# Optimization experiments

Hardware: AMD Instinct MI355X
Metric: run time of the kernel (lower is better)

The kernel has to match this reference:

```python
import jax, jax.numpy as jnp
import numpy as np

HIDDEN = 1024
HEADS = 16
HEAD_DIM = HIDDEN // HEADS


def setup_inputs() -> dict:
    key = jax.random.key(0)
    ks = jax.random.split(key, 4)
    B, S, H = 2, 2048, HIDDEN
    scale = 1.0 / np.sqrt(H)
    return {
        "inputs": jax.random.normal(ks[0], (B, S, H), dtype=jnp.float32),
        "mask": jnp.ones((B, S), dtype=jnp.int32),
        "Wq": jax.random.normal(ks[1], (H, H), dtype=jnp.float32) * scale,
        "bq": jnp.zeros((H,), dtype=jnp.float32),
        "Wk": jax.random.normal(ks[2], (H, H), dtype=jnp.float32) * scale,
        "bk": jnp.zeros((H,), dtype=jnp.float32),
        "Wv": jax.random.normal(ks[3], (H, H), dtype=jnp.float32) * scale,
        "bv": jnp.zeros((H,), dtype=jnp.float32),
    }


def _split_heads(x, B, S):
    # [B,S,H] -> [B,heads,S,head_dim]
    return x.reshape(B, S, HEADS, HEAD_DIM).transpose(0, 2, 1, 3)


def reference(inputs, mask, Wq, bq, Wk, bk, Wv, bv):
    B, S, H = inputs.shape
    q = _split_heads(inputs @ Wq.T + bq, B, S)
    k = _split_heads(inputs @ Wk.T + bk, B, S)
    v = _split_heads(inputs @ Wv.T + bv, B, S)
    scores = jnp.einsum("bhqd,bhkd->bhqk", q, k) / jnp.sqrt(
        jnp.asarray(HEAD_DIM, dtype=inputs.dtype))
    # mask broadcast [B,1,1,S]; zeros -> -inf
    scores = jnp.where(mask[:, None, None, :] == 0, -jnp.inf, scores)
    attn = jax.nn.softmax(scores, axis=-1)
    context = jnp.einsum("bhqk,bhkd->bhqd", attn, v)
    return context.transpose(0, 2, 1, 3).reshape(B, S, H)
```

## Files before the change

kernel.cpp:

```cpp
#include <hip/hip_runtime.h>
#include <hip/hip_fp16.h>

constexpr int S_LEN  = 2048;
constexpr int HID    = 1024;
constexpr int HEADS  = 16;
constexpr int HDIM   = 64;
constexpr int BATCH  = 2;
constexpr int BH     = BATCH * HEADS;
constexpr int M_ROWS = BATCH * S_LEN;

typedef _Float16 half8  __attribute__((ext_vector_type(8)));
typedef _Float16 half4v __attribute__((ext_vector_type(4)));
typedef _Float16 half2v __attribute__((ext_vector_type(2)));
typedef float    f32x4  __attribute__((ext_vector_type(4)));
typedef float    f32x16 __attribute__((ext_vector_type(16)));

constexpr float EXP2_OFF = -11.541560327111707f;
constexpr float Q_SCALE  = 0.18033688011112042f;

__global__ __launch_bounds__(256) void cvt_kernel(
    const float* __restrict__ X,  const float* __restrict__ Wq,
    const float* __restrict__ Wk, const float* __restrict__ Wv,
    const int* __restrict__ mask,
    _Float16* __restrict__ Xh,  _Float16* __restrict__ Wqh,
    _Float16* __restrict__ Wkh, _Float16* __restrict__ Wvh,
    float* __restrict__ maskF)
{
    const int blk = blockIdx.x;
    if (blk >= 3584) {
        const int loc = blk - 3584;
        const size_t e = ((size_t)loc * 256 + threadIdx.x) * 8;
        #pragma unroll
        for (int i = 0; i < 8; ++i)
            maskF[e + i] = mask[e + i] ? EXP2_OFF : -1.0e30f;
        return;
    }
    const float* src; _Float16* dst; int loc;
    if (blk < 2048)      { src = X;  dst = Xh;  loc = blk; }
    else if (blk < 2560) { src = Wq; dst = Wqh; loc = blk - 2048; }
    else if (blk < 3072) { src = Wk; dst = Wkh; loc = blk - 2560; }
    else                 { src = Wv; dst = Wvh; loc = blk - 3072; }
    const size_t e = ((size_t)loc * 256 + threadIdx.x) * 8;
    float4 a = *reinterpret_cast<const float4*>(&src[e]);
    float4 b = *reinterpret_cast<const float4*>(&src[e + 4]);
    half8 h = { (_Float16)a.x, (_Float16)a.y, (_Float16)a.z, (_Float16)a.w,
                (_Float16)b.x, (_Float16)b.y, (_Float16)b.z, (_Float16)b.w };
    *reinterpret_cast<half8*>(&dst[e]) = h;
}

__device__ __forceinline__ void async_cp16(_Float16* lds, const _Float16* g) {
    __builtin_amdgcn_global_load_lds(
        (const __attribute__((address_space(1))) void*)g,
        (__attribute__((address_space(3))) void*)lds, 16, 0, 0);
}

__global__ __launch_bounds__(256) void qkv_proj_kernel(
    const _Float16* __restrict__ Xh,
    const _Float16* __restrict__ Wqh, const _Float16* __restrict__ Wkh,
    const _Float16* __restrict__ Wvh,
    const float* __restrict__ bq, const float* __restrict__ bk,
    const float* __restrict__ bv,
    _Float16* __restrict__ Qo, _Float16* __restrict__ Ko,
    _Float16* __restrict__ Vt)
{
    const int mode = blockIdx.z;
    const _Float16* W    = (mode == 0) ? Wqh : (mode == 1) ? Wkh : Wvh;
    const float*    bias = (mode == 0) ? bq  : (mode == 1) ? bk  : bv;

    const int m0 = blockIdx.x * 128, n0 = blockIdx.y * 128;
    const int tid = threadIdx.x, wave = tid >> 6, lane = tid & 63;
    const int l31 = lane & 31, kg = lane >> 5;

    __shared__ _Float16 SMEM[18432];

    f32x16 acc[2][2];
    #pragma unroll
    for (int mt = 0; mt < 2; ++mt)
        #pragma unroll
        for (int nt = 0; nt < 2; ++nt)
            #pragma unroll
            for (int i = 0; i < 16; ++i) acc[mt][nt][i] = 0.f;

    const int wm = (wave & 1) * 64, wn = (wave >> 1) * 64;

    const int srow = tid >> 2, spos = tid & 3;
    auto stage = [&](int k0, int b) {
        _Float16* Asb = SMEM + b * 8192;
        _Float16* Bsb = Asb + 4096;
        #pragma unroll
        for (int j = 0; j < 2; ++j) {
            const int row = srow + j * 64;
            const int sch = spos ^ (row & 3);
            async_cp16(&Asb[j * 2048 + tid * 8],
                       &Xh[(size_t)(m0 + row) * HID + k0 + sch * 8]);
            async_cp16(&Bsb[j * 2048 + tid * 8],
                       &W [(size_t)(n0 + row) * HID + k0 + sch * 8]);
        }
    };

    stage(0, 0);
    int buf = 0;

    for (int k0 = 0; k0 < HID; k0 += 32) {
        __syncthreads();
        if (k0 + 32 < HID) stage(k0 + 32, buf ^ 1);
        _Float16* Asb = SMEM + buf * 8192;
        _Float16* Bsb = Asb + 4096;

        #pragma unroll
        for (int c = 0; c < 2; ++c) {
            const int k8 = c * 2 + kg;
            half8 af[2], bf[2];
            #pragma unroll
            for (int mt = 0; mt < 2; ++mt) {
                const int row = wm + mt * 32 + l31;
                af[mt] = *reinterpret_cast<const half8*>(
                    &Asb[row * 32 + ((k8 ^ (row & 3)) * 8)]);
            }
            #pragma unroll
            for (int nt = 0; nt < 2; ++nt) {
                const int row = wn + nt * 32 + l31;
                bf[nt] = *reinterpret_cast<const half8*>(
                    &Bsb[row * 32 + ((k8 ^ (row & 3)) * 8)]);
            }
            #pragma unroll
            for (int mt = 0; mt < 2; ++mt)
                #pragma unroll
                for (int nt = 0; nt < 2; ++nt)
                    acc[mt][nt] = __builtin_amdgcn_mfma_f32_32x32x16_f16(
                        af[mt], bf[nt], acc[mt][nt], 0, 0, 0);
        }
        buf ^= 1;
    }
    __syncthreads();

    _Float16* T = SMEM + wave * 4608;

    const int nn  = n0 + wn;
    const int hh  = nn >> 6;
    const int mm  = m0 + wm;
    const int bb  = mm >> 11;
    const int bhv = bb * HEADS + hh;
    const int s0  = mm & 2047;
    const int rowg = lane >> 3, chunk = lane & 7;

    if (mode < 2) {
        _Float16* Out = (mode == 0) ? Qo : Ko;
        #pragma unroll
        for (int nt = 0; nt < 2; ++nt) {
            const int col = nt * 32 + l31;
            float bias_n = bias[nn + col];
            #pragma unroll
            for (int mt = 0; mt < 2; ++mt)
                #pragma unroll
                for (int r = 0; r < 16; ++r) {
                    const int row_l = (r & 3) + 8 * (r >> 2) + 4 * kg;
                    float v = acc[mt][nt][r] + bias_n;
                    if (mode == 0) v *= Q_SCALE;
                    T[(mt * 32 + row_l) * 72 + col] = (_Float16)v;
                }
        }
        asm volatile("s_waitcnt lgkmcnt(0)" ::: "memory");
        #pragma unroll
        for (int j = 0; j < 8; ++j) {
            const int sr = j * 8 + rowg;
            half8 v = *reinterpret_cast<const half8*>(&T[sr * 72 + chunk * 8]);
            *reinterpret_cast<half8*>(
                &Out[((size_t)bhv * S_LEN + s0 + sr) * HDIM + chunk * 8]) = v;
        }
    } else {
        #pragma unroll
        for (int nt = 0; nt < 2; ++nt) {
            const int col = nt * 32 + l31;
            const float bias_n = bias[nn + col];
            #pragma unroll
            for (int mt = 0; mt < 2; ++mt)
                #pragma unroll
                for (int rg = 0; rg < 4; ++rg) {
                    half4v t = { (_Float16)(acc[mt][nt][rg * 4 + 0] + bias_n),
                                 (_Float16)(acc[mt][nt][rg * 4 + 1] + bias_n),
                                 (_Float16)(acc[mt][nt][rg * 4 + 2] + bias_n),
                                 (_Float16)(acc[mt][nt][rg * 4 + 3] + bias_n) };
                    const int s_off = mt * 32 + 8 * rg + 4 * kg;
                    *reinterpret_cast<half4v*>(&T[col * 72 + s_off]) = t;
                }
        }
        asm volatile("s_waitcnt lgkmcnt(0)" ::: "memory");
        #pragma unroll
        for (int j = 0; j < 8; ++j) {
            const int dr = j * 8 + rowg;
            half8 v = *reinterpret_cast<const half8*>(&T[dr * 72 + chunk * 8]);
            *reinterpret_cast<half8*>(
                &Vt[((size_t)bhv * HDIM + dr) * S_LEN + s0 + chunk * 8]) = v;
        }
    }
}

__global__ __launch_bounds__(512) void attn_kernel(
    const _Float16* __restrict__ Q, const _Float16* __restrict__ K,
    const _Float16* __restrict__ Vt, const float* __restrict__ maskF,
    float* __restrict__ Out)
{
    const int id    = blockIdx.x;
    const int xcd   = id & 7, local = id >> 3;
    const int bh    = xcd * 4 + (local & 3);
    const int qt    = local >> 2;
    const int b = bh >> 4, h = bh & 15;
    const int tid = threadIdx.x, wave = tid >> 6, lane = tid & 63;
    const int l15 = lane & 15, quad = lane >> 4;

    __shared__ _Float16 Ks[2][64 * 64];
    __shared__ _Float16 Vs[2][64 * 64];
    __shared__ _Float16 Ps[8][16][68];

    const _Float16* Qb = Q  + (size_t)bh * S_LEN * HDIM;
    const _Float16* Kb = K  + (size_t)bh * S_LEN * HDIM;
    const _Float16* Vb = Vt + (size_t)bh * HDIM * S_LEN;
    const float*    mb = maskF + b * S_LEN;

    const int qrow = qt * 128 + wave * 16 + l15;
    half8 qf[2];
    qf[0] = *reinterpret_cast<const half8*>(&Qb[(size_t)qrow * HDIM + quad * 8]);
    qf[1] = *reinterpret_cast<const half8*>(&Qb[(size_t)qrow * HDIM + 32 + quad * 8]);

    f32x4 acc[4];
    #pragma unroll
    for (int mt = 0; mt < 4; ++mt) acc[mt] = (f32x4){0.f, 0.f, 0.f, 0.f};
    float den = 0.f;

    const int srow_t  = tid >> 3;
    const int schunk  = (tid & 7) ^ (srow_t & 7);
    auto stage = [&](int kb, int buf) {
        async_cp16(&Ks[buf][tid * 8],
                   &Kb[(size_t)(kb + srow_t) * HDIM + schunk * 8]);
        async_cp16(&Vs[buf][tid * 8],
                   &Vb[(size_t)srow_t * S_LEN + kb + schunk * 8]);
    };

    stage(0, 0);
    int buf = 0;
    const int rsw = (l15 & 7);

    for (int kb = 0; kb < S_LEN; kb += 64) {
        __syncthreads();
        if (kb + 64 < S_LEN) stage(kb + 64, buf ^ 1);

        float4 m4[4];
        #pragma unroll
        for (int nt = 0; nt < 4; ++nt)
            m4[nt] = *reinterpret_cast<const float4*>(&mb[kb + nt * 16 + quad * 4]);

        half8 kf[2][4];
        #pragma unroll
        for (int c = 0; c < 2; ++c)
            #pragma unroll
            for (int nt = 0; nt < 4; ++nt)
                kf[c][nt] = *reinterpret_cast<const half8*>(
                    &Ks[buf][(nt * 16 + l15) * 64 + ((c * 4 + quad) ^ rsw) * 8]);
        f32x4 sc[4];
        #pragma unroll
        for (int nt = 0; nt < 4; ++nt) sc[nt] = (f32x4){0.f, 0.f, 0.f, 0.f};
        #pragma unroll
        for (int c = 0; c < 2; ++c)
            #pragma unroll
            for (int nt = 0; nt < 4; ++nt)
                sc[nt] = __builtin_amdgcn_mfma_f32_16x16x32_f16(
                    kf[c][nt], qf[c], sc[nt], 0, 0, 0);

        half8 vf[2][4];
        #pragma unroll
        for (int c = 0; c < 2; ++c)
            #pragma unroll
            for (int mt = 0; mt < 4; ++mt)
                vf[c][mt] = *reinterpret_cast<const half8*>(
                    &Vs[buf][(mt * 16 + l15) * 64 + ((c * 4 + quad) ^ rsw) * 8]);

        #pragma unroll
        for (int nt = 0; nt < 4; ++nt) {
            float p0 = __builtin_amdgcn_exp2f(sc[nt][0] + m4[nt].x);
            float p1 = __builtin_amdgcn_exp2f(sc[nt][1] + m4[nt].y);
            float p2 = __builtin_amdgcn_exp2f(sc[nt][2] + m4[nt].z);
            float p3 = __builtin_amdgcn_exp2f(sc[nt][3] + m4[nt].w);
            den += (p0 + p1) + (p2 + p3);
            half2v lo = __builtin_bit_cast(half2v, __builtin_amdgcn_cvt_pkrtz(p0, p1));
            half2v hi = __builtin_bit_cast(half2v, __builtin_amdgcn_cvt_pkrtz(p2, p3));
            half4v pk = { lo[0], lo[1], hi[0], hi[1] };
            *reinterpret_cast<half4v*>(&Ps[wave][l15][nt * 16 + quad * 4]) = pk;
        }
        asm volatile("s_waitcnt lgkmcnt(0)" ::: "memory");

        #pragma unroll
        for (int c = 0; c < 2; ++c) {
            half4v plo = *reinterpret_cast<const half4v*>(
                &Ps[wave][l15][c * 32 + quad * 8]);
            half4v phi = *reinterpret_cast<const half4v*>(
                &Ps[wave][l15][c * 32 + quad * 8 + 4]);
            half8 pf = { plo[0], plo[1], plo[2], plo[3],
                         phi[0], phi[1], phi[2], phi[3] };
            #pragma unroll
            for (int mt = 0; mt < 4; ++mt)
                acc[mt] = __builtin_amdgcn_mfma_f32_16x16x32_f16(
                    vf[c][mt], pf, acc[mt], 0, 0, 0);
        }
        buf ^= 1;
    }

    den += __shfl_xor(den, 16, 64);
    den += __shfl_xor(den, 32, 64);
    const float inv = 1.0f / den;

    float* orow = Out + ((size_t)(b * S_LEN + qrow)) * HID + h * HDIM;
    #pragma unroll
    for (int mt = 0; mt < 4; ++mt) {
        float4 o = { acc[mt][0] * inv, acc[mt][1] * inv,
                     acc[mt][2] * inv, acc[mt][3] * inv };
        *reinterpret_cast<float4*>(&orow[mt * 16 + quad * 4]) = o;
    }
}

extern "C" void kernel_launch(void* const* d_in, const int* in_sizes, int n_in,
                              void* d_out, int out_size, void* d_ws, size_t ws_size,
                              hipStream_t stream) {
    const float* X  = (const float*)d_in[0];
    const int*   mk = (const int*)  d_in[1];
    const float* Wq = (const float*)d_in[2];
    const float* bq = (const float*)d_in[3];
    const float* Wk = (const float*)d_in[4];
    const float* bk = (const float*)d_in[5];
    const float* Wv = (const float*)d_in[6];
    const float* bv = (const float*)d_in[7];
    float* out = (float*)d_out;

    _Float16* Xh  = (_Float16*)d_ws;
    _Float16* Wqh = Xh  + (size_t)M_ROWS * HID;
    _Float16* Wkh = Wqh + (size_t)HID * HID;
    _Float16* Wvh = Wkh + (size_t)HID * HID;
    _Float16* Q   = Wvh + (size_t)HID * HID;
    _Float16* K   = Q   + (size_t)BH * S_LEN * HDIM;
    _Float16* Vt  = K   + (size_t)BH * S_LEN * HDIM;
    float*    maskF = (float*)(Vt + (size_t)BH * S_LEN * HDIM);

    cvt_kernel<<<3586, 256, 0, stream>>>(X, Wq, Wk, Wv, mk, Xh, Wqh, Wkh, Wvh, maskF);

    dim3 gp(M_ROWS / 128, HID / 128, 3);
    qkv_proj_kernel<<<gp, 256, 0, stream>>>(Xh, Wqh, Wkh, Wvh, bq, bk, bv, Q, K, Vt);

    attn_kernel<<<512, 512, 0, stream>>>(Q, K, Vt, maskF, out);
}
```

Measured before the change: 173.6 us.

## Split attention over two key halves with a separate combine kernel

Splits the key dimension of attention into two halves, doubling the grid to 1024 blocks. One half writes an unnormalized fp16 partial to workspace (reusing the Xh buffer) and the other writes fp32 directly into the output, and each half stores its row denominators. A new reduce kernel adds the partials and normalizes. The K/V staging is made single-buffered with two barriers per iteration, which gives up copy/compute overlap in exchange for more resident blocks and a smaller LDS footprint. The change adds an extra launch, extra traffic for the partial results, and fp16 rounding of one partial.

```diff
diff --git a/kernel.cpp b/kernel.cpp
--- a/kernel.cpp
+++ b/kernel.cpp
@@ -196,27 +196,30 @@
     }
 }
 
-__global__ __launch_bounds__(512) void attn_kernel(
+__global__ __launch_bounds__(512, 8) void attn_kernel(
     const _Float16* __restrict__ Q, const _Float16* __restrict__ K,
     const _Float16* __restrict__ Vt, const float* __restrict__ maskF,
+    _Float16* __restrict__ Oa, float* __restrict__ den_out,
     float* __restrict__ Out)
 {
     const int id    = blockIdx.x;
     const int xcd   = id & 7, local = id >> 3;
     const int bh    = xcd * 4 + (local & 3);
-    const int qt    = local >> 2;
+    const int qt    = (local >> 2) & 15;
+    const int kh    = local >> 6;
     const int b = bh >> 4, h = bh & 15;
     const int tid = threadIdx.x, wave = tid >> 6, lane = tid & 63;
     const int l15 = lane & 15, quad = lane >> 4;
 
-    __shared__ _Float16 Ks[2][64 * 64];
-    __shared__ _Float16 Vs[2][64 * 64];
+    __shared__ _Float16 Ks[64 * 64];
+    __shared__ _Float16 Vs[64 * 64];
     __shared__ _Float16 Ps[8][16][68];
 
     const _Float16* Qb = Q  + (size_t)bh * S_LEN * HDIM;
     const _Float16* Kb = K  + (size_t)bh * S_LEN * HDIM;
     const _Float16* Vb = Vt + (size_t)bh * HDIM * S_LEN;
     const float*    mb = maskF + b * S_LEN;
+    const int       k0 = kh * 1024;
 
     const int qrow = qt * 128 + wave * 16 + l15;
     half8 qf[2];
@@ -230,20 +233,13 @@
 
     const int srow_t  = tid >> 3;
     const int schunk  = (tid & 7) ^ (srow_t & 7);
-    auto stage = [&](int kb, int buf) {
-        async_cp16(&Ks[buf][tid * 8],
-                   &Kb[(size_t)(kb + srow_t) * HDIM + schunk * 8]);
-        async_cp16(&Vs[buf][tid * 8],
-                   &Vb[(size_t)srow_t * S_LEN + kb + schunk * 8]);
-    };
-
-    stage(0, 0);
-    int buf = 0;
     const int rsw = (l15 & 7);
 
-    for (int kb = 0; kb < S_LEN; kb += 64) {
+    for (int it = 0; it < 16; ++it) {
+        const int kb = k0 + it * 64;
+        async_cp16(&Ks[tid * 8], &Kb[(size_t)(kb + srow_t) * HDIM + schunk * 8]);
+        async_cp16(&Vs[tid * 8], &Vb[(size_t)srow_t * S_LEN + kb + schunk * 8]);
         __syncthreads();
-        if (kb + 64 < S_LEN) stage(kb + 64, buf ^ 1);
 
         float4 m4[4];
         #pragma unroll
@@ -256,7 +252,7 @@
             #pragma unroll
             for (int nt = 0; nt < 4; ++nt)
                 kf[c][nt] = *reinterpret_cast<const half8*>(
-                    &Ks[buf][(nt * 16 + l15) * 64 + ((c * 4 + quad) ^ rsw) * 8]);
+                    &Ks[(nt * 16 + l15) * 64 + ((c * 4 + quad) ^ rsw) * 8]);
         f32x4 sc[4];
         #pragma unroll
         for (int nt = 0; nt < 4; ++nt) sc[nt] = (f32x4){0.f, 0.f, 0.f, 0.f};
@@ -273,7 +269,7 @@
             #pragma unroll
             for (int mt = 0; mt < 4; ++mt)
                 vf[c][mt] = *reinterpret_cast<const half8*>(
-                    &Vs[buf][(mt * 16 + l15) * 64 + ((c * 4 + quad) ^ rsw) * 8]);
+                    &Vs[(mt * 16 + l15) * 64 + ((c * 4 + quad) ^ rsw) * 8]);
 
         #pragma unroll
         for (int nt = 0; nt < 4; ++nt) {
@@ -302,20 +298,51 @@
                 acc[mt] = __builtin_amdgcn_mfma_f32_16x16x32_f16(
                     vf[c][mt], pf, acc[mt], 0, 0, 0);
         }
-        buf ^= 1;
+        __syncthreads();
     }
 
     den += __shfl_xor(den, 16, 64);
     den += __shfl_xor(den, 32, 64);
-    const float inv = 1.0f / den;
-
-    float* orow = Out + ((size_t)(b * S_LEN + qrow)) * HID + h * HDIM;
-    #pragma unroll
-    for (int mt = 0; mt < 4; ++mt) {
-        float4 o = { acc[mt][0] * inv, acc[mt][1] * inv,
-                     acc[mt][2] * inv, acc[mt][3] * inv };
-        *reinterpret_cast<float4*>(&orow[mt * 16 + quad * 4]) = o;
-    }
+    if (quad == 0)
+        den_out[kh * (BH * S_LEN) + bh * S_LEN + qrow] = den;
+
+    if (kh == 0) {
+        _Float16* orow = Oa + ((size_t)bh * S_LEN + qrow) * HDIM;
+        #pragma unroll
+        for (int mt = 0; mt < 4; ++mt) {
+            half4v o = { (_Float16)acc[mt][0], (_Float16)acc[mt][1],
+                         (_Float16)acc[mt][2], (_Float16)acc[mt][3] };
+            *reinterpret_cast<half4v*>(&orow[mt * 16 + quad * 4]) = o;
+        }
+    } else {
+        float* orow = Out + ((size_t)(b * S_LEN + qrow)) * HID + h * HDIM;
+        #pragma unroll
+        for (int mt = 0; mt < 4; ++mt) {
+            float4 o = { acc[mt][0], acc[mt][1], acc[mt][2], acc[mt][3] };
+            *reinterpret_cast<float4*>(&orow[mt * 16 + quad * 4]) = o;
+        }
+    }
+}
+
+__global__ __launch_bounds__(256) void reduce_kernel(
+    const _Float16* __restrict__ Oa, const float* __restrict__ den,
+    float* __restrict__ Out)
+{
+    const int gid  = blockIdx.x * 256 + threadIdx.x;
+    const int d4   = gid & 15;
+    const int qrow = (gid >> 4) & 2047;
+    const int bh   = gid >> 15;
+    const int b = bh >> 4, h = bh & 15;
+
+    const size_t oa_off = ((size_t)bh * S_LEN + qrow) * HDIM + d4 * 4;
+    half4v a = *reinterpret_cast<const half4v*>(&Oa[oa_off]);
+    const float inv = 1.0f / (den[bh * S_LEN + qrow] +
+                              den[BH * S_LEN + bh * S_LEN + qrow]);
+    float* op = Out + ((size_t)(b * S_LEN + qrow)) * HID + h * HDIM + d4 * 4;
+    float4 pb = *reinterpret_cast<const float4*>(op);
+    float4 o = { (pb.x + (float)a[0]) * inv, (pb.y + (float)a[1]) * inv,
+                 (pb.z + (float)a[2]) * inv, (pb.w + (float)a[3]) * inv };
+    *reinterpret_cast<float4*>(op) = o;
 }
 
 extern "C" void kernel_launch(void* const* d_in, const int* in_sizes, int n_in,
@@ -331,19 +358,23 @@
     const float* bv = (const float*)d_in[7];
     float* out = (float*)d_out;
 
-    _Float16* Xh  = (_Float16*)d_ws;
+    _Float16* Q   = (_Float16*)d_ws;
+    _Float16* K   = Q  + (size_t)BH * S_LEN * HDIM;
+    _Float16* Vt  = K  + (size_t)BH * S_LEN * HDIM;
+    float*    maskF = (float*)(Vt + (size_t)BH * S_LEN * HDIM);
+    float*    den   = maskF + BATCH * S_LEN;
+    _Float16* Xh  = (_Float16*)(den + 2 * BH * S_LEN);
     _Float16* Wqh = Xh  + (size_t)M_ROWS * HID;
     _Float16* Wkh = Wqh + (size_t)HID * HID;
     _Float16* Wvh = Wkh + (size_t)HID * HID;
-    _Float16* Q   = Wvh + (size_t)HID * HID;
-    _Float16* K   = Q   + (size_t)BH * S_LEN * HDIM;
-    _Float16* Vt  = K   + (size_t)BH * S_LEN * HDIM;
-    float*    maskF = (float*)(Vt + (size_t)BH * S_LEN * HDIM);
+    _Float16* Oa  = Xh;
 
     cvt_kernel<<<3586, 256, 0, stream>>>(X, Wq, Wk, Wv, mk, Xh, Wqh, Wkh, Wvh, maskF);
 
     dim3 gp(M_ROWS / 128, HID / 128, 3);
     qkv_proj_kernel<<<gp, 256, 0, stream>>>(Xh, Wqh, Wkh, Wvh, bq, bk, bv, Q, K, Vt);
 
-    attn_kernel<<<512, 512, 0, stream>>>(Q, K, Vt, maskF, out);
-}
+    attn_kernel<<<1024, 512, 0, stream>>>(Q, K, Vt, maskF, Oa, den, out);
+
+    reduce_kernel<<<4096, 256, 0, stream>>>(Oa, den, out);
+}
```

Result: slower. 318.2 us (+83.3%).
